# Performance work log

Measured on AMD Instinct MI355X. Metric: run time of the kernel, lower is better.

The kernel has to match this reference:

```python
import jax, jax.numpy as jnp
import numpy as np

SIGMA = 5.0
THRESH = 0.1

def setup_inputs() -> dict:
    key = jax.random.key(0)
    k1, k2, k3 = jax.random.split(key, 3)
    B, N, H, W = 8, 20, 512, 512
    y_pred = jax.random.normal(k1, (B, 1, H, W), dtype=jnp.float32)
    point_labels = jax.random.randint(k2, (B, N), 0, 2, dtype=jnp.int32)
    point_coords = jax.random.uniform(k3, (B, N, 2), dtype=jnp.float32)
    return {"y_pred": y_pred, "point_labels": point_labels, "point_coords": point_coords}


def _soft_labels(point_labels, point_coords, H, W):
    # Replicates the sequential overwrite-scatter: for each pixel, the LAST
    B, N = point_labels.shape
    yc = point_coords[..., 0] * H  # (B, N)
    xc = point_coords[..., 1] * W  # (B, N)
    yg = jnp.arange(H, dtype=jnp.float32)
    xg = jnp.arange(W, dtype=jnp.float32)
    # (B, N, H, W) squared distance from each point to each pixel
    dist_sq = (yg[None, None, :, None] - yc[:, :, None, None]) ** 2 \
            + (xg[None, None, None, :] - xc[:, :, None, None]) ** 2
    mask = jnp.exp(-dist_sq / (2.0 * SIGMA ** 2)) > THRESH  # (B, N, H, W)
    n_idx = jnp.arange(N, dtype=jnp.int32)[None, :, None, None]
    last = jnp.max(jnp.where(mask, n_idx, -1), axis=1)  # (B, H, W); -1 = no point
    valid = last >= 0
    labels = jnp.take_along_axis(
        point_labels.astype(jnp.float32)[:, :, None], last.clip(0).reshape(B, 1, -1)[:, 0][:, None, :].swapaxes(1, 2)[..., 0][:, None, :], axis=1
    ) if False else point_labels.astype(jnp.float32)[jnp.arange(B)[:, None, None], last.clip(0)]
    return labels, valid


def reference(y_pred, point_labels, point_coords):
    B, _, H, W = y_pred.shape
    labels, valid = _soft_labels(point_labels, point_coords, H, W)
    logits = y_pred[:, 0]  # (B, H, W)
    # numerically-stable BCE with logits
    bce = jnp.maximum(logits, 0.0) - logits * labels + jnp.log1p(jnp.exp(-jnp.abs(logits)))
    cnt = valid.sum()
    loss = jnp.where(cnt > 0,
                     jnp.sum(bce * valid) / jnp.maximum(cnt, 1).astype(jnp.float32),
                     jnp.float32(0.0))
    return loss
```

## Files before the change

### kernel.cpp

```cpp
#include <hip/hip_runtime.h>
#include <math.h>


#define R2_THRESH 115.12925464970229f
#define HW 512
#define NPTS 20
#define NBLOCKS 512
#define MAGIC 0x5F3C9A17u
#define MAGIC2 0x5F3C9A175F3C9A17ull

__global__ __launch_bounds__(256)
void pce_kernel(const float* __restrict__ y_pred,
                const int* __restrict__ point_labels,
                const float* __restrict__ point_coords,
                float* __restrict__ slots,
                unsigned* __restrict__ flags,
                float* __restrict__ out) {
    const int bid   = blockIdx.x;
    const int b     = bid >> 6;
    const int chunk = bid & 63;
    const int y0    = chunk * 8;
    const int tid   = threadIdx.x;
    const int r     = tid >> 5;
    const int lane  = tid & 31;

    __shared__ float s_xc[8][NPTS], s_lim[8][NPTS], s_lab[8][NPTS];

    float xlo = INFINITY, xhi = -INFINITY;
    if (lane < NPTS) {
        float2 cc = ((const float2*)point_coords)[b * NPTS + lane];
        float yc  = cc.x * (float)HW;
        float xc  = cc.y * (float)HW;
        float dy  = (float)(y0 + r) - yc;
        float lim = R2_THRESH - dy * dy;
        s_xc[r][lane]  = xc;
        s_lim[r][lane] = lim;
        s_lab[r][lane] = (float)point_labels[b * NPTS + lane];
        if (lim > 0.0f) {
            float s = sqrtf(lim);
            xlo = xc - s;
            xhi = xc + s;
        }
    }
    #pragma unroll
    for (int off = 16; off > 0; off >>= 1) {
        xlo = fminf(xlo, __shfl_xor(xlo, off, 32));
        xhi = fmaxf(xhi, __shfl_xor(xhi, off, 32));
    }
    const int x0 = (int)fminf(fmaxf(floorf(xlo), 0.0f), 512.0f);
    const int x1 = (int)fminf(fmaxf(ceilf(xhi), -1.0f), 511.0f);
    __syncthreads();

    float sum = 0.0f, cnt = 0.0f;
    const float* row = y_pred + (size_t)b * HW * HW + (size_t)(y0 + r) * HW;
    for (int px = x0 + lane; px <= x1; px += 32) {
        float l = row[px];
        const float fx = (float)px;
        float lab = 0.0f;
        bool  valid = false;
        #pragma unroll
        for (int k = 0; k < NPTS; ++k) {
            float dx = fx - s_xc[r][k];
            if (dx * dx < s_lim[r][k]) { lab = s_lab[r][k]; valid = true; }
        }
        if (valid) {
            sum += fmaxf(l, 0.0f) - l * lab + log1pf(expf(-fabsf(l)));
            cnt += 1.0f;
        }
    }

    #pragma unroll
    for (int off = 32; off > 0; off >>= 1) {
        sum += __shfl_down(sum, off, 64);
        cnt += __shfl_down(cnt, off, 64);
    }
    __shared__ float rs[4], rc[4];
    if ((tid & 63) == 0) { rs[tid >> 6] = sum; rc[tid >> 6] = cnt; }
    __syncthreads();
    if (tid == 0) {
        float S = rs[0] + rs[1] + rs[2] + rs[3];
        float C = rc[0] + rc[1] + rc[2] + rc[3];
        __hip_atomic_store(&slots[bid * 2 + 0], S, __ATOMIC_RELAXED, __HIP_MEMORY_SCOPE_AGENT);
        __hip_atomic_store(&slots[bid * 2 + 1], C, __ATOMIC_RELAXED, __HIP_MEMORY_SCOPE_AGENT);
        __hip_atomic_store(&flags[bid], MAGIC, __ATOMIC_RELEASE, __HIP_MEMORY_SCOPE_AGENT);
    }
    if (bid != 0) return;

    {
        unsigned long long f = 0;
        unsigned long long* fp = (unsigned long long*)&flags[2 * tid];
        do {
            f = __hip_atomic_load(fp, __ATOMIC_ACQUIRE, __HIP_MEMORY_SCOPE_AGENT);
            if (f != MAGIC2) __builtin_amdgcn_s_sleep(1);
        } while (f != MAGIC2);
    }

    {
        float s0 = __hip_atomic_load(&slots[4 * tid + 0], __ATOMIC_RELAXED, __HIP_MEMORY_SCOPE_AGENT);
        float c0 = __hip_atomic_load(&slots[4 * tid + 1], __ATOMIC_RELAXED, __HIP_MEMORY_SCOPE_AGENT);
        float s1 = __hip_atomic_load(&slots[4 * tid + 2], __ATOMIC_RELAXED, __HIP_MEMORY_SCOPE_AGENT);
        float c1 = __hip_atomic_load(&slots[4 * tid + 3], __ATOMIC_RELAXED, __HIP_MEMORY_SCOPE_AGENT);
        float S = s0 + s1;
        float C = c0 + c1;
        #pragma unroll
        for (int off = 32; off > 0; off >>= 1) {
            S += __shfl_down(S, off, 64);
            C += __shfl_down(C, off, 64);
        }
        if ((tid & 63) == 0) { rs[tid >> 6] = S; rc[tid >> 6] = C; }
        __syncthreads();
        if (tid == 0) {
            float SS = rs[0] + rs[1] + rs[2] + rs[3];
            float CC = rc[0] + rc[1] + rc[2] + rc[3];
            out[0] = (CC > 0.0f) ? (SS / CC) : 0.0f;
        }
        __hip_atomic_store(&flags[2 * tid + 0], 0u, __ATOMIC_RELAXED, __HIP_MEMORY_SCOPE_AGENT);
        __hip_atomic_store(&flags[2 * tid + 1], 0u, __ATOMIC_RELAXED, __HIP_MEMORY_SCOPE_AGENT);
    }
}

extern "C" void kernel_launch(void* const* d_in, const int* in_sizes, int n_in,
                              void* d_out, int out_size, void* d_ws, size_t ws_size,
                              hipStream_t stream) {
    const float* y_pred       = (const float*)d_in[0];
    const int*   point_labels = (const int*)d_in[1];
    const float* point_coords = (const float*)d_in[2];
    float*       out          = (float*)d_out;

    char* w = (char*)d_ws;
    float*    slots = (float*)(w);
    unsigned* flags = (unsigned*)(w + 4096);

    pce_kernel<<<NBLOCKS, 256, 0, stream>>>(y_pred, point_labels, point_coords,
                                            slots, flags, out);
}
```

Baseline: 19.62 us.

## Prefetch full row strip into LDS with float4 loads; pack slot pairs into 64-bit

Each block now loads its entire 8-row strip of logits with vectorized float4 loads issued before the point setup, stages it in shared memory, and the masked pixel loop reads from LDS instead of doing scattered global loads over only the covered x-range. This hides global latency behind the setup and shuffles, but reads every pixel rather than just the covered span, adding 16 KB of LDS per block. The per-block partial sum and count are also packed into a single 64-bit atomic store and load, removing a few memory operations in the final reduction.

```diff
diff --git a/kernel.cpp b/kernel.cpp
--- a/kernel.cpp
+++ b/kernel.cpp
@@ -13,18 +13,24 @@
 void pce_kernel(const float* __restrict__ y_pred,
                 const int* __restrict__ point_labels,
                 const float* __restrict__ point_coords,
-                float* __restrict__ slots,
+                unsigned long long* __restrict__ slots,
                 unsigned* __restrict__ flags,
                 float* __restrict__ out) {
-    const int bid   = blockIdx.x;
-    const int b     = bid >> 6;
-    const int chunk = bid & 63;
-    const int y0    = chunk * 8;
-    const int tid   = threadIdx.x;
-    const int r     = tid >> 5;
-    const int lane  = tid & 31;
+    const int bid  = blockIdx.x;
+    const int b    = bid >> 6;
+    const int y0   = (bid & 63) * 8;
+    const int tid  = threadIdx.x;
+    const int r    = tid >> 5;
+    const int lane = tid & 31;
 
+    __shared__ float s_strip[8][HW];
     __shared__ float s_xc[8][NPTS], s_lim[8][NPTS], s_lab[8][NPTS];
+
+    const float4* grow = (const float4*)(y_pred + (size_t)b * HW * HW + (size_t)(y0 + r) * HW);
+    float4 v0 = grow[lane];
+    float4 v1 = grow[lane + 32];
+    float4 v2 = grow[lane + 64];
+    float4 v3 = grow[lane + 96];
 
     float xlo = INFINITY, xhi = -INFINITY;
     if (lane < NPTS) {
@@ -49,12 +55,19 @@
     }
     const int x0 = (int)fminf(fmaxf(floorf(xlo), 0.0f), 512.0f);
     const int x1 = (int)fminf(fmaxf(ceilf(xhi), -1.0f), 511.0f);
+
+    {
+        float4* dst = (float4*)&s_strip[r][0];
+        dst[lane]      = v0;
+        dst[lane + 32] = v1;
+        dst[lane + 64] = v2;
+        dst[lane + 96] = v3;
+    }
     __syncthreads();
 
     float sum = 0.0f, cnt = 0.0f;
-    const float* row = y_pred + (size_t)b * HW * HW + (size_t)(y0 + r) * HW;
     for (int px = x0 + lane; px <= x1; px += 32) {
-        float l = row[px];
+        float l = s_strip[r][px];
         const float fx = (float)px;
         float lab = 0.0f;
         bool  valid = false;
@@ -80,8 +93,9 @@
     if (tid == 0) {
         float S = rs[0] + rs[1] + rs[2] + rs[3];
         float C = rc[0] + rc[1] + rc[2] + rc[3];
-        __hip_atomic_store(&slots[bid * 2 + 0], S, __ATOMIC_RELAXED, __HIP_MEMORY_SCOPE_AGENT);
-        __hip_atomic_store(&slots[bid * 2 + 1], C, __ATOMIC_RELAXED, __HIP_MEMORY_SCOPE_AGENT);
+        unsigned long long w = ((unsigned long long)__float_as_uint(C) << 32)
+                             | (unsigned long long)__float_as_uint(S);
+        __hip_atomic_store(&slots[bid], w, __ATOMIC_RELAXED, __HIP_MEMORY_SCOPE_AGENT);
         __hip_atomic_store(&flags[bid], MAGIC, __ATOMIC_RELEASE, __HIP_MEMORY_SCOPE_AGENT);
     }
     if (bid != 0) return;
@@ -96,12 +110,12 @@
     }
 
     {
-        float s0 = __hip_atomic_load(&slots[4 * tid + 0], __ATOMIC_RELAXED, __HIP_MEMORY_SCOPE_AGENT);
-        float c0 = __hip_atomic_load(&slots[4 * tid + 1], __ATOMIC_RELAXED, __HIP_MEMORY_SCOPE_AGENT);
-        float s1 = __hip_atomic_load(&slots[4 * tid + 2], __ATOMIC_RELAXED, __HIP_MEMORY_SCOPE_AGENT);
-        float c1 = __hip_atomic_load(&slots[4 * tid + 3], __ATOMIC_RELAXED, __HIP_MEMORY_SCOPE_AGENT);
-        float S = s0 + s1;
-        float C = c0 + c1;
+        unsigned long long w0 = __hip_atomic_load(&slots[2 * tid + 0], __ATOMIC_RELAXED, __HIP_MEMORY_SCOPE_AGENT);
+        unsigned long long w1 = __hip_atomic_load(&slots[2 * tid + 1], __ATOMIC_RELAXED, __HIP_MEMORY_SCOPE_AGENT);
+        float S = __uint_as_float((unsigned)(w0 & 0xffffffffull))
+                + __uint_as_float((unsigned)(w1 & 0xffffffffull));
+        float C = __uint_as_float((unsigned)(w0 >> 32))
+                + __uint_as_float((unsigned)(w1 >> 32));
         #pragma unroll
         for (int off = 32; off > 0; off >>= 1) {
             S += __shfl_down(S, off, 64);
@@ -128,8 +142,8 @@
     float*       out          = (float*)d_out;
 
     char* w = (char*)d_ws;
-    float*    slots = (float*)(w);
-    unsigned* flags = (unsigned*)(w + 4096);
+    unsigned long long* slots = (unsigned long long*)(w);
+    unsigned*           flags = (unsigned*)(w + 4096);
 
     pce_kernel<<<NBLOCKS, 256, 0, stream>>>(y_pred, point_labels, point_coords,
                                             slots, flags, out);
```

New measurement: 19.62 us, median of 2. No clear change (+0.0%).
